# Optimization experiments

Hardware: AMD Instinct MI355X
Metric: run time of the kernel (lower is better)

The kernel has to match this reference:

```python
import jax, jax.numpy as jnp
import numpy as np

B, S, D, H = 4, 2048, 1024, 16
DK = D // H
THETA = 10000.0


def _rope(x, token_positions):
    # x: [b, h, s, d_k]; token_positions: [s] int
    half = x.shape[-1] // 2
    freqs = 1.0 / (THETA ** (2.0 * jnp.arange(half, dtype=jnp.float32) / x.shape[-1]))
    angles = token_positions.astype(jnp.float32)[:, None] * freqs[None, :]  # [s, half]
    cos, sin = jnp.cos(angles), jnp.sin(angles)
    x1 = x[..., 0::2]  # interleaved pairing: (d/2, 2)
    x2 = x[..., 1::2]
    r1 = x1 * cos - x2 * sin
    r2 = x2 * cos + x1 * sin
    return jnp.stack([r1, r2], axis=-1).reshape(x.shape)


def setup_inputs() -> dict:
    key = jax.random.key(0)
    ks = jax.random.split(key, 5)
    std_io = np.sqrt(2.0 / (D + D)).astype(np.float32)
    return {
        "x": jax.random.normal(ks[0], (B, S, D), dtype=jnp.float32),
        "token_positions": jnp.arange(S, dtype=jnp.int32),
        "Wq": jax.random.normal(ks[1], (D, D), dtype=jnp.float32) * std_io,
        "Wk": jax.random.normal(ks[2], (D, D), dtype=jnp.float32) * std_io,
        "Wv": jax.random.normal(ks[3], (D, D), dtype=jnp.float32) * std_io,
        "Wo": jax.random.normal(ks[4], (D, D), dtype=jnp.float32) * std_io,
    }


def reference(x, token_positions, Wq, Wk, Wv, Wo):
    b, s, d = x.shape
    # Linear uses W: [out, in] -> y = x @ W.T
    def proj(W):
        y = jnp.einsum('bsd,od->bso', x, W)
        return y.reshape(b, s, H, DK).transpose(0, 2, 1, 3)  # [b,h,s,dk]
    q, k, v = proj(Wq), proj(Wk), proj(Wv)
    q = _rope(q, token_positions)
    k = _rope(k, token_positions)
    scores = jnp.einsum('bhqd,bhkd->bhqk', q, k) / jnp.sqrt(jnp.float32(DK))
    causal = jnp.tril(jnp.ones((s, s), dtype=bool))
    scores = jnp.where(causal, scores, -jnp.inf)
    attn = jax.nn.softmax(scores, axis=-1)
    out = jnp.einsum('bhqk,bhkd->bhqd', attn, v)
    out = out.transpose(0, 2, 1, 3).reshape(b, s, d)
    return jnp.einsum('bsd,od->bso', out, Wo)
```

## Files before the change

### kernel.cpp

```cpp
#include <hip/hip_runtime.h>
#include <math.h>

#define B_ 4
#define S_ 2048
#define D_ 1024
#define H_ 16
#define DK_ 64
#define SCALE_ 0.125f
#define THETA_ 10000.0f
#define LOG2E_ 1.44269504f
#define THR_ 8.0f

typedef unsigned short ushort_t;
typedef __attribute__((ext_vector_type(8))) short bf16x8;
typedef __attribute__((ext_vector_type(4))) float f32x4;

__device__ __forceinline__ ushort_t f2bf(float f) {
    union { float f; unsigned u; } v; v.f = f;
    unsigned r = (v.u + 0x7FFFu + ((v.u >> 16) & 1u)) >> 16;
    return (ushort_t)r;
}

__device__ __forceinline__ unsigned permpk(float lo, float hi) {
    return __builtin_amdgcn_perm(__float_as_uint(hi), __float_as_uint(lo), 0x07060302u);
}

__device__ __forceinline__ int vswz(int row) { return (row & 7) ^ ((row >> 3) & 3); }

#define GLOAD_LDS16(gptr, lptr)                                                   \
    __builtin_amdgcn_global_load_lds(                                             \
        (const __attribute__((address_space(1))) unsigned int*)(gptr),            \
        (__attribute__((address_space(3))) unsigned int*)(lptr), 16, 0, 0)

__global__ __launch_bounds__(256) void cast_f32_bf16(const float* __restrict__ in,
                                                     ushort_t* __restrict__ out, int n) {
    int i = (blockIdx.x * 256 + threadIdx.x) * 4;
    if (i >= n) return;
    float4 v = *reinterpret_cast<const float4*>(in + i);
    unsigned lo = (unsigned)f2bf(v.x) | ((unsigned)f2bf(v.y) << 16);
    unsigned hi = (unsigned)f2bf(v.z) | ((unsigned)f2bf(v.w) << 16);
    uint2 u; u.x = lo; u.y = hi;
    *reinterpret_cast<uint2*>(out + i) = u;
}

__global__ __launch_bounds__(256) void build_rope(const int* __restrict__ pos,
                                                  float2* __restrict__ tab) {
    int i = blockIdx.x * 256 + threadIdx.x;
    int s = i >> 5, p = i & 31;
    float freq = powf(THETA_, -2.0f * (float)p / 64.0f);
    float a = (float)pos[s] * freq;
    tab[i] = make_float2(cosf(a), sinf(a));
}

template <int MODE>
__global__ __launch_bounds__(256) void gemm_bf16(const ushort_t* __restrict__ A,
                                                 const ushort_t* __restrict__ W,
                                                 const float2* __restrict__ tab,
                                                 float qscale,
                                                 float* __restrict__ outF,
                                                 ushort_t* __restrict__ outB) {
    __shared__ ushort_t Asl[128 * 32];
    __shared__ ushort_t Bsl[128 * 32];

    const int t = threadIdx.x;
    const int lane = t & 63;
    const int w = t >> 6;
    const int lr = lane & 15;
    const int lg = lane >> 4;

    const int bid = blockIdx.x;
    const int swz = (bid & 7) * 64 + (bid >> 3);
    const int m0 = (swz >> 3) * 128;
    const int n0 = (swz & 7) * 128;

    const int wr = w >> 1;
    const int wc = w & 1;

    f32x4 acc[4][4] = {};

    for (int k0 = 0; k0 < D_; k0 += 32) {
#pragma unroll
        for (int i = 0; i < 2; ++i) {
            const int off = w * 2048 + i * 1024 + lane * 16;
            const int row = off >> 6;
            const int col = (off & 63) >> 1;
            GLOAD_LDS16(A + (size_t)(m0 + row) * D_ + k0 + col, Asl + (w * 1024 + i * 512));
            GLOAD_LDS16(W + (size_t)(n0 + row) * D_ + k0 + col, Bsl + (w * 1024 + i * 512));
        }
        __syncthreads();

        bf16x8 af[4], bfr[4];
#pragma unroll
        for (int x = 0; x < 4; ++x) {
            af[x]  = *reinterpret_cast<const bf16x8*>(&Asl[(wr * 64 + x * 16 + lr) * 32 + lg * 8]);
            bfr[x] = *reinterpret_cast<const bf16x8*>(&Bsl[(wc * 64 + x * 16 + lr) * 32 + lg * 8]);
        }
#pragma unroll
        for (int mi = 0; mi < 4; ++mi)
#pragma unroll
            for (int ni = 0; ni < 4; ++ni)
                acc[mi][ni] = __builtin_amdgcn_mfma_f32_16x16x32_bf16(af[mi], bfr[ni], acc[mi][ni], 0, 0, 0);
        __syncthreads();
    }

#pragma unroll
    for (int mi = 0; mi < 4; ++mi) {
#pragma unroll
        for (int r = 0; r < 4; ++r) {
            const int m = m0 + wr * 64 + mi * 16 + lg * 4 + r;
            const int bb = m >> 11;
            const int s = m & (S_ - 1);
#pragma unroll
            for (int ni = 0; ni < 4; ++ni) {
                const int n = n0 + wc * 64 + ni * 16 + lr;
                float v = acc[mi][ni][r];
                if (MODE == 0) {
                    outF[(size_t)m * D_ + n] = v;
                } else {
                    const int h = n >> 6, dk = n & 63;
                    if (MODE == 2) {
                        v *= qscale;
                        const float2 cs = tab[s * 32 + (dk >> 1)];
                        const float part = __shfl_xor(v, 1, 64);
                        v = (dk & 1) ? fmaf(v, cs.x, part * cs.y)
                                     : fmaf(v, cs.x, -part * cs.y);
                    }
                    outB[(((size_t)bb * H_ + h) * S_ + s) * DK_ + dk] = f2bf(v);
                }
            }
        }
    }
}

__global__ __launch_bounds__(512) void attn_mfma(const ushort_t* __restrict__ Q,
                                                 const ushort_t* __restrict__ K,
                                                 const ushort_t* __restrict__ V,
                                                 ushort_t* __restrict__ O) {
    __shared__ ushort_t Ks[2][64 * 64];
    __shared__ ushort_t Vt[64 * 64];
    __shared__ ushort_t Pl[128 * 64];

    const int t = threadIdx.x;
    const int lane = t & 63;
    const int w = t >> 6;
    const int lr = lane & 15;
    const int lg = lane >> 4;

    const int bid = blockIdx.x;
    const int swz = (bid & 7) * 64 + (bid >> 3);
    const int bh = swz >> 3;
    const int p  = swz & 7;

    const ushort_t* Kbase = K + (size_t)bh * S_ * DK_;
    const ushort_t* Vbase = V + (size_t)bh * S_ * DK_;
    const int bb = bh >> 4, h = bh & 15;

    const int krow = t >> 3;
    const int kc16 = (t & 7) ^ (krow & 7);
    const int dk8 = (t & 7) * 8;
    const int kv2 = ((t >> 3) & 31) * 2;

    bf16x8 ones;
#pragma unroll
    for (int j = 0; j < 8; ++j) ones[j] = (short)0x3F80;

    bf16x8 vpre0, vpre1;

    for (int ph = 0; ph < 2; ++ph) {
        const int qt = ph ? (15 - p) : p;
        const int q0 = qt * 128;
        const int nt = 2 * qt + 2;

        const ushort_t* Qbase = Q + ((size_t)bh * S_ + q0 + w * 16) * DK_;
        bf16x8 qf[2];
#pragma unroll
        for (int kf = 0; kf < 2; ++kf)
            qf[kf] = *reinterpret_cast<const bf16x8*>(
                Qbase + (size_t)lr * DK_ + kf * 32 + lg * 8);

        f32x4 acc[4] = {};
        f32x4 accl = {};
        float mrow = -INFINITY;

        GLOAD_LDS16(Kbase + (size_t)krow * DK_ + kc16 * 8, &Ks[0][t * 8]);
        if (t < 256) {
            const ushort_t* Vsrc = Vbase + (size_t)kv2 * DK_ + dk8;
            vpre0 = *reinterpret_cast<const bf16x8*>(Vsrc);
            vpre1 = *reinterpret_cast<const bf16x8*>(Vsrc + DK_);
        }
        __syncthreads();

        int cur = 0;
        for (int kt = 0; kt < nt; ++kt) {
            if (t < 256) {
                const unsigned* aw = reinterpret_cast<const unsigned*>(&vpre0);
                const unsigned* bw = reinterpret_cast<const unsigned*>(&vpre1);
#pragma unroll
                for (int j = 0; j < 8; ++j) {
                    const int row = dk8 + j;
                    const unsigned sel = (j & 1) ? 0x07060302u : 0x05040100u;
                    const unsigned pk = __builtin_amdgcn_perm(bw[j >> 1], aw[j >> 1], sel);
                    *reinterpret_cast<unsigned*>(
                        (char*)Vt + row * 128 + ((kv2 * 2) ^ (vswz(row) << 4))) = pk;
                }
            }
            __syncthreads();

            if (kt + 1 < nt) {
                const ushort_t* Ksrc = Kbase + (size_t)(kt + 1) * 64 * DK_;
                GLOAD_LDS16(Ksrc + (size_t)krow * DK_ + kc16 * 8, &Ks[cur ^ 1][t * 8]);
                if (t < 256) {
                    const ushort_t* Vsrc = Vbase + (size_t)((kt + 1) * 64 + kv2) * DK_ + dk8;
                    vpre0 = *reinterpret_cast<const bf16x8*>(Vsrc);
                    vpre1 = *reinterpret_cast<const bf16x8*>(Vsrc + DK_);
                }
            }

            bf16x8 kb[4][2];
#pragma unroll
            for (int nf = 0; nf < 4; ++nf)
#pragma unroll
                for (int kf = 0; kf < 2; ++kf)
                    kb[nf][kf] = *reinterpret_cast<const bf16x8*>(
                        (char*)Ks[cur] + (nf * 16 + lr) * 128 + (((kf * 4 + lg) ^ (lr & 7)) << 4));

            f32x4 sT[4];
#pragma unroll
            for (int nf = 0; nf < 4; ++nf) {
                f32x4 z = {};
                z = __builtin_amdgcn_mfma_f32_16x16x32_bf16(kb[nf][0], qf[0], z, 0, 0, 0);
                z = __builtin_amdgcn_mfma_f32_16x16x32_bf16(kb[nf][1], qf[1], z, 0, 0, 0);
                sT[nf] = z;
            }

            if (kt >= nt - 2) {
                const int q = q0 + w * 16 + lr;
#pragma unroll
                for (int nf = 0; nf < 4; ++nf)
#pragma unroll
                    for (int r = 0; r < 4; ++r) {
                        const int kv = kt * 64 + nf * 16 + lg * 4 + r;
                        if (kv > q) sT[nf][r] = -INFINITY;
                    }
            }

            {
                float m4 = -INFINITY;
#pragma unroll
                for (int nf = 0; nf < 4; ++nf)
#pragma unroll
                    for (int r = 0; r < 4; ++r) m4 = fmaxf(m4, sT[nf][r]);
                m4 = fmaxf(m4, __shfl_xor(m4, 16, 64));
                m4 = fmaxf(m4, __shfl_xor(m4, 32, 64));
                if (m4 > mrow + THR_) {
                    const float corr = __builtin_amdgcn_exp2f(mrow - m4);
                    mrow = m4;
#pragma unroll
                    for (int r = 0; r < 4; ++r) accl[r] *= corr;
#pragma unroll
                    for (int df = 0; df < 4; ++df)
#pragma unroll
                        for (int r = 0; r < 4; ++r) acc[df][r] *= corr;
                }
            }

            const int prow = w * 16 + lr;
            char* prowp = (char*)Pl + prow * 128;
#pragma unroll
            for (int nf = 0; nf < 4; ++nf) {
                const float p0 = __builtin_amdgcn_exp2f(sT[nf][0] - mrow);
                const float p1 = __builtin_amdgcn_exp2f(sT[nf][1] - mrow);
                const float p2 = __builtin_amdgcn_exp2f(sT[nf][2] - mrow);
                const float p3 = __builtin_amdgcn_exp2f(sT[nf][3] - mrow);
                uint2 pk;
                pk.x = permpk(p0, p1);
                pk.y = permpk(p2, p3);
                const int chunk = (nf * 2 + (lg >> 1)) ^ (lr & 7);
                *reinterpret_cast<uint2*>(prowp + (chunk << 4) + (lg & 1) * 8) = pk;
            }

            bf16x8 pfr[2];
#pragma unroll
            for (int kf = 0; kf < 2; ++kf)
                pfr[kf] = *reinterpret_cast<const bf16x8*>(
                    (char*)Pl + prow * 128 + (((kf * 4 + lg) ^ (lr & 7)) << 4));

            bf16x8 vtf[4][2];
#pragma unroll
            for (int df = 0; df < 4; ++df)
#pragma unroll
                for (int kf = 0; kf < 2; ++kf)
                    vtf[df][kf] = *reinterpret_cast<const bf16x8*>(
                        (char*)Vt + (df * 16 + lr) * 128 + (((kf * 4 + lg) ^ vswz(df * 16 + lr)) << 4));

#pragma unroll
            for (int kf = 0; kf < 2; ++kf)
                accl = __builtin_amdgcn_mfma_f32_16x16x32_bf16(ones, pfr[kf], accl, 0, 0, 0);
#pragma unroll
            for (int df = 0; df < 4; ++df)
#pragma unroll
                for (int kf = 0; kf < 2; ++kf)
                    acc[df] = __builtin_amdgcn_mfma_f32_16x16x32_bf16(vtf[df][kf], pfr[kf], acc[df], 0, 0, 0);

            __syncthreads();
            cur ^= 1;
        }

        const float inv = 1.0f / accl[0];
        const int q = q0 + w * 16 + lr;
        ushort_t* Orow = O + ((size_t)bb * S_ + q) * D_ + h * DK_;
#pragma unroll
        for (int df = 0; df < 4; ++df) {
            unsigned lo = (unsigned)f2bf(acc[df][0] * inv) | ((unsigned)f2bf(acc[df][1] * inv) << 16);
            unsigned hi = (unsigned)f2bf(acc[df][2] * inv) | ((unsigned)f2bf(acc[df][3] * inv) << 16);
            *reinterpret_cast<unsigned*>(Orow + df * 16 + lg * 4)     = lo;
            *reinterpret_cast<unsigned*>(Orow + df * 16 + lg * 4 + 2) = hi;
        }
    }
}

extern "C" void kernel_launch(void* const* d_in, const int* in_sizes, int n_in,
                              void* d_out, int out_size, void* d_ws, size_t ws_size,
                              hipStream_t stream) {
    const float* x  = (const float*)d_in[0];
    const int*   tp = (const int*)d_in[1];
    const float* Wq = (const float*)d_in[2];
    const float* Wk = (const float*)d_in[3];
    const float* Wv = (const float*)d_in[4];
    const float* Wo = (const float*)d_in[5];
    float* out = (float*)d_out;

    char* ws = (char*)d_ws;
    ushort_t* Xb  = (ushort_t*)(ws);
    ushort_t* Wqb = (ushort_t*)(ws + (16ull << 20));
    ushort_t* Wkb = (ushort_t*)(ws + (18ull << 20));
    ushort_t* Wvb = (ushort_t*)(ws + (20ull << 20));
    ushort_t* Wob = (ushort_t*)(ws + (22ull << 20));
    ushort_t* Qb  = (ushort_t*)(ws + (24ull << 20));
    ushort_t* Kb  = (ushort_t*)(ws + (40ull << 20));
    ushort_t* Vb  = (ushort_t*)(ws + (56ull << 20));
    ushort_t* Ao  = (ushort_t*)(ws + (72ull << 20));
    float2*   tab = (float2*)(ws + (88ull << 20));

    const int NX = B_ * S_ * D_;
    const int NW = D_ * D_;
    cast_f32_bf16<<<NX / 1024, 256, 0, stream>>>(x, Xb, NX);
    cast_f32_bf16<<<NW / 1024, 256, 0, stream>>>(Wq, Wqb, NW);
    cast_f32_bf16<<<NW / 1024, 256, 0, stream>>>(Wk, Wkb, NW);
    cast_f32_bf16<<<NW / 1024, 256, 0, stream>>>(Wv, Wvb, NW);
    cast_f32_bf16<<<NW / 1024, 256, 0, stream>>>(Wo, Wob, NW);
    build_rope<<<(S_ * 32) / 256, 256, 0, stream>>>(tp, tab);

    gemm_bf16<2><<<512, 256, 0, stream>>>(Xb, Wqb, tab, SCALE_ * LOG2E_, nullptr, Qb);
    gemm_bf16<2><<<512, 256, 0, stream>>>(Xb, Wkb, tab, 1.0f, nullptr, Kb);
    gemm_bf16<1><<<512, 256, 0, stream>>>(Xb, Wvb, tab, 1.0f, nullptr, Vb);

    attn_mfma<<<512, 512, 0, stream>>>(Qb, Kb, Vb, Ao);

    gemm_bf16<0><<<512, 256, 0, stream>>>(Ao, Wob, tab, 1.0f, out, nullptr);
}
```

Measured before the change: 196.2 us.

## Widen attention KV tile to 128 and fuse cast kernels into one launch

The attention kernel now processes 128 keys per iteration instead of 64, halving the number of loop iterations, barriers and online-softmax rescales. All 512 threads now take part in K and V loading, and the P·V MFMAs load fragments on the fly. Separately, the five f32-to-bf16 cast launches are merged into a single kernel, which relies on the weight buffers being contiguous in the workspace (2 MB apart). The larger LDS footprint (about 64 KB) and higher register pressure may reduce occupancy.

```diff
diff --git a/kernel.cpp b/kernel.cpp
--- a/kernel.cpp
+++ b/kernel.cpp
@@ -32,15 +32,32 @@
         (const __attribute__((address_space(1))) unsigned int*)(gptr),            \
         (__attribute__((address_space(3))) unsigned int*)(lptr), 16, 0, 0)
 
-__global__ __launch_bounds__(256) void cast_f32_bf16(const float* __restrict__ in,
-                                                     ushort_t* __restrict__ out, int n) {
-    int i = (blockIdx.x * 256 + threadIdx.x) * 4;
-    if (i >= n) return;
-    float4 v = *reinterpret_cast<const float4*>(in + i);
+__global__ __launch_bounds__(256) void cast_all(const float* __restrict__ x,
+                                                const float* __restrict__ W0,
+                                                const float* __restrict__ W1,
+                                                const float* __restrict__ W2,
+                                                const float* __restrict__ W3,
+                                                ushort_t* __restrict__ Xb,
+                                                ushort_t* __restrict__ Wb) {
+    const int bid = blockIdx.x;
+    const float* src;
+    ushort_t* dst;
+    int i;
+    if (bid < 8192) {
+        src = x; dst = Xb;
+        i = bid * 1024 + threadIdx.x * 4;
+    } else {
+        const int seg = (bid - 8192) >> 10;
+        const int lb  = (bid - 8192) & 1023;
+        src = (seg == 0) ? W0 : (seg == 1) ? W1 : (seg == 2) ? W2 : W3;
+        dst = Wb + (size_t)seg * (D_ * D_);
+        i = lb * 1024 + threadIdx.x * 4;
+    }
+    float4 v = *reinterpret_cast<const float4*>(src + i);
     unsigned lo = (unsigned)f2bf(v.x) | ((unsigned)f2bf(v.y) << 16);
     unsigned hi = (unsigned)f2bf(v.z) | ((unsigned)f2bf(v.w) << 16);
     uint2 u; u.x = lo; u.y = hi;
-    *reinterpret_cast<uint2*>(out + i) = u;
+    *reinterpret_cast<uint2*>(dst + i) = u;
 }
 
 __global__ __launch_bounds__(256) void build_rope(const int* __restrict__ pos,
@@ -136,9 +153,9 @@
                                                  const ushort_t* __restrict__ K,
                                                  const ushort_t* __restrict__ V,
                                                  ushort_t* __restrict__ O) {
-    __shared__ ushort_t Ks[2][64 * 64];
-    __shared__ ushort_t Vt[64 * 64];
-    __shared__ ushort_t Pl[128 * 64];
+    __shared__ ushort_t Ks[2][128 * 64];
+    __shared__ ushort_t Vt[64 * 128];
+    __shared__ ushort_t Pl[128 * 128];
 
     const int t = threadIdx.x;
     const int lane = t & 63;
@@ -155,10 +172,8 @@
     const ushort_t* Vbase = V + (size_t)bh * S_ * DK_;
     const int bb = bh >> 4, h = bh & 15;
 
-    const int krow = t >> 3;
-    const int kc16 = (t & 7) ^ (krow & 7);
     const int dk8 = (t & 7) * 8;
-    const int kv2 = ((t >> 3) & 31) * 2;
+    const int kv2 = (t >> 3) * 2;
 
     bf16x8 ones;
 #pragma unroll
@@ -169,7 +184,7 @@
     for (int ph = 0; ph < 2; ++ph) {
         const int qt = ph ? (15 - p) : p;
         const int q0 = qt * 128;
-        const int nt = 2 * qt + 2;
+        const int nt = qt + 1;
 
         const ushort_t* Qbase = Q + ((size_t)bh * S_ + q0 + w * 16) * DK_;
         bf16x8 qf[2];
@@ -182,8 +197,14 @@
         f32x4 accl = {};
         float mrow = -INFINITY;
 
-        GLOAD_LDS16(Kbase + (size_t)krow * DK_ + kc16 * 8, &Ks[0][t * 8]);
-        if (t < 256) {
+#pragma unroll
+        for (int it = 0; it < 2; ++it) {
+            const int slot = it * 512 + t;
+            const int row = slot >> 3;
+            const int c16 = (slot & 7) ^ (row & 7);
+            GLOAD_LDS16(Kbase + (size_t)row * DK_ + c16 * 8, &Ks[0][slot * 8]);
+        }
+        {
             const ushort_t* Vsrc = Vbase + (size_t)kv2 * DK_ + dk8;
             vpre0 = *reinterpret_cast<const bf16x8*>(Vsrc);
             vpre1 = *reinterpret_cast<const bf16x8*>(Vsrc + DK_);
@@ -192,7 +213,7 @@
 
         int cur = 0;
         for (int kt = 0; kt < nt; ++kt) {
-            if (t < 256) {
+            {
                 const unsigned* aw = reinterpret_cast<const unsigned*>(&vpre0);
                 const unsigned* bw = reinterpret_cast<const unsigned*>(&vpre1);
 #pragma unroll
@@ -201,45 +222,45 @@
                     const unsigned sel = (j & 1) ? 0x07060302u : 0x05040100u;
                     const unsigned pk = __builtin_amdgcn_perm(bw[j >> 1], aw[j >> 1], sel);
                     *reinterpret_cast<unsigned*>(
-                        (char*)Vt + row * 128 + ((kv2 * 2) ^ (vswz(row) << 4))) = pk;
+                        (char*)Vt + row * 256 + ((kv2 * 2) ^ (vswz(row) << 4))) = pk;
                 }
             }
             __syncthreads();
 
             if (kt + 1 < nt) {
-                const ushort_t* Ksrc = Kbase + (size_t)(kt + 1) * 64 * DK_;
-                GLOAD_LDS16(Ksrc + (size_t)krow * DK_ + kc16 * 8, &Ks[cur ^ 1][t * 8]);
-                if (t < 256) {
-                    const ushort_t* Vsrc = Vbase + (size_t)((kt + 1) * 64 + kv2) * DK_ + dk8;
-                    vpre0 = *reinterpret_cast<const bf16x8*>(Vsrc);
-                    vpre1 = *reinterpret_cast<const bf16x8*>(Vsrc + DK_);
-                }
-            }
-
-            bf16x8 kb[4][2];
-#pragma unroll
-            for (int nf = 0; nf < 4; ++nf)
-#pragma unroll
-                for (int kf = 0; kf < 2; ++kf)
-                    kb[nf][kf] = *reinterpret_cast<const bf16x8*>(
-                        (char*)Ks[cur] + (nf * 16 + lr) * 128 + (((kf * 4 + lg) ^ (lr & 7)) << 4));
-
-            f32x4 sT[4];
-#pragma unroll
-            for (int nf = 0; nf < 4; ++nf) {
+                const ushort_t* Ksrc = Kbase + (size_t)(kt + 1) * 128 * DK_;
+#pragma unroll
+                for (int it = 0; it < 2; ++it) {
+                    const int slot = it * 512 + t;
+                    const int row = slot >> 3;
+                    const int c16 = (slot & 7) ^ (row & 7);
+                    GLOAD_LDS16(Ksrc + (size_t)row * DK_ + c16 * 8, &Ks[cur ^ 1][slot * 8]);
+                }
+                const ushort_t* Vsrc = Vbase + (size_t)((kt + 1) * 128 + kv2) * DK_ + dk8;
+                vpre0 = *reinterpret_cast<const bf16x8*>(Vsrc);
+                vpre1 = *reinterpret_cast<const bf16x8*>(Vsrc + DK_);
+            }
+
+            f32x4 sT[8];
+#pragma unroll
+            for (int nf = 0; nf < 8; ++nf) {
+                bf16x8 kb0 = *reinterpret_cast<const bf16x8*>(
+                    (char*)Ks[cur] + (nf * 16 + lr) * 128 + (((0 + lg) ^ (lr & 7)) << 4));
+                bf16x8 kb1 = *reinterpret_cast<const bf16x8*>(
+                    (char*)Ks[cur] + (nf * 16 + lr) * 128 + (((4 + lg) ^ (lr & 7)) << 4));
                 f32x4 z = {};
-                z = __builtin_amdgcn_mfma_f32_16x16x32_bf16(kb[nf][0], qf[0], z, 0, 0, 0);
-                z = __builtin_amdgcn_mfma_f32_16x16x32_bf16(kb[nf][1], qf[1], z, 0, 0, 0);
+                z = __builtin_amdgcn_mfma_f32_16x16x32_bf16(kb0, qf[0], z, 0, 0, 0);
+                z = __builtin_amdgcn_mfma_f32_16x16x32_bf16(kb1, qf[1], z, 0, 0, 0);
                 sT[nf] = z;
             }
 
-            if (kt >= nt - 2) {
+            if (kt == nt - 1) {
                 const int q = q0 + w * 16 + lr;
 #pragma unroll
-                for (int nf = 0; nf < 4; ++nf)
+                for (int nf = 0; nf < 8; ++nf)
 #pragma unroll
                     for (int r = 0; r < 4; ++r) {
-                        const int kv = kt * 64 + nf * 16 + lg * 4 + r;
+                        const int kv = kt * 128 + nf * 16 + lg * 4 + r;
                         if (kv > q) sT[nf][r] = -INFINITY;
                     }
             }
@@ -247,7 +268,7 @@
             {
                 float m4 = -INFINITY;
 #pragma unroll
-                for (int nf = 0; nf < 4; ++nf)
+                for (int nf = 0; nf < 8; ++nf)
 #pragma unroll
                     for (int r = 0; r < 4; ++r) m4 = fmaxf(m4, sT[nf][r]);
                 m4 = fmaxf(m4, __shfl_xor(m4, 16, 64));
@@ -265,9 +286,9 @@
             }
 
             const int prow = w * 16 + lr;
-            char* prowp = (char*)Pl + prow * 128;
-#pragma unroll
-            for (int nf = 0; nf < 4; ++nf) {
+            char* prowp = (char*)Pl + prow * 256;
+#pragma unroll
+            for (int nf = 0; nf < 8; ++nf) {
                 const float p0 = __builtin_amdgcn_exp2f(sT[nf][0] - mrow);
                 const float p1 = __builtin_amdgcn_exp2f(sT[nf][1] - mrow);
                 const float p2 = __builtin_amdgcn_exp2f(sT[nf][2] - mrow);
@@ -279,28 +300,19 @@
                 *reinterpret_cast<uint2*>(prowp + (chunk << 4) + (lg & 1) * 8) = pk;
             }
 
-            bf16x8 pfr[2];
-#pragma unroll
-            for (int kf = 0; kf < 2; ++kf)
-                pfr[kf] = *reinterpret_cast<const bf16x8*>(
-                    (char*)Pl + prow * 128 + (((kf * 4 + lg) ^ (lr & 7)) << 4));
-
-            bf16x8 vtf[4][2];
-#pragma unroll
-            for (int df = 0; df < 4; ++df)
-#pragma unroll
-                for (int kf = 0; kf < 2; ++kf)
-                    vtf[df][kf] = *reinterpret_cast<const bf16x8*>(
-                        (char*)Vt + (df * 16 + lr) * 128 + (((kf * 4 + lg) ^ vswz(df * 16 + lr)) << 4));
-
-#pragma unroll
-            for (int kf = 0; kf < 2; ++kf)
-                accl = __builtin_amdgcn_mfma_f32_16x16x32_bf16(ones, pfr[kf], accl, 0, 0, 0);
-#pragma unroll
-            for (int df = 0; df < 4; ++df)
-#pragma unroll
-                for (int kf = 0; kf < 2; ++kf)
-                    acc[df] = __builtin_amdgcn_mfma_f32_16x16x32_bf16(vtf[df][kf], pfr[kf], acc[df], 0, 0, 0);
+#pragma unroll
+            for (int kf = 0; kf < 4; ++kf) {
+                bf16x8 pf = *reinterpret_cast<const bf16x8*>(
+                    prowp + (((kf * 4 + lg) ^ (lr & 7)) << 4));
+                accl = __builtin_amdgcn_mfma_f32_16x16x32_bf16(ones, pf, accl, 0, 0, 0);
+#pragma unroll
+                for (int df = 0; df < 4; ++df) {
+                    const int vrow = df * 16 + lr;
+                    bf16x8 vf = *reinterpret_cast<const bf16x8*>(
+                        (char*)Vt + vrow * 256 + (((kf * 4 + lg) ^ vswz(vrow)) << 4));
+                    acc[df] = __builtin_amdgcn_mfma_f32_16x16x32_bf16(vf, pf, acc[df], 0, 0, 0);
+                }
+            }
 
             __syncthreads();
             cur ^= 1;
@@ -342,13 +354,7 @@
     ushort_t* Ao  = (ushort_t*)(ws + (72ull << 20));
     float2*   tab = (float2*)(ws + (88ull << 20));
 
-    const int NX = B_ * S_ * D_;
-    const int NW = D_ * D_;
-    cast_f32_bf16<<<NX / 1024, 256, 0, stream>>>(x, Xb, NX);
-    cast_f32_bf16<<<NW / 1024, 256, 0, stream>>>(Wq, Wqb, NW);
-    cast_f32_bf16<<<NW / 1024, 256, 0, stream>>>(Wk, Wkb, NW);
-    cast_f32_bf16<<<NW / 1024, 256, 0, stream>>>(Wv, Wvb, NW);
-    cast_f32_bf16<<<NW / 1024, 256, 0, stream>>>(Wo, Wob, NW);
+    cast_all<<<8192 + 4096, 256, 0, stream>>>(x, Wq, Wk, Wv, Wo, Xb, Wqb);
     build_rope<<<(S_ * 32) / 256, 256, 0, stream>>>(tp, tab);
 
     gemm_bf16<2><<<512, 256, 0, stream>>>(Xb, Wqb, tab, SCALE_ * LOG2E_, nullptr, Qb);
```

Result: no change. 198.1 us (+1.0%).
